# Optimization experiments

Hardware: AMD Instinct MI355X
Metric: run time of the kernel (lower is better)

## Reference

```python
import jax, jax.numpy as jnp
import numpy as np
import math
from jax import lax

N_SCALES = 5
ORDER = 2
INC, OUTC = 20, 40
MIN = np.arange(N_SCALES) * 0.2          # per-scale band lower edges [0,.2,.4,.6,.8]
MAX = MIN + 0.2                          # per-scale band upper edges [.2,...,1.0]
SIGMA0 = (MIN + MAX) / 2.0               # sigma at init (scales=0 -> tanh=0)
FS = [int(math.ceil(2.0 * s)) for s in SIGMA0]  # static half filter sizes [1,1,1,2,2]
MAXK = 2 * max(FS) + 1                   # padded kernel size (5)


def _hermite_derivs(x, sigma, order):
    # n-th Gaussian derivative: (-1/(sigma*sqrt2))^n * H_n(x/(sigma*sqrt2)) * g(x)
    g = jnp.exp(-(x ** 2) / (2.0 * sigma ** 2))
    g = g / jnp.sum(g)  # unit-sum normalized Gaussian envelope
    u = x / (sigma * math.sqrt(2.0))
    H = [jnp.ones_like(u), 2.0 * u]
    for n in range(1, order):
        H.append(2.0 * u * H[n] - 2.0 * n * H[n - 1])
    return [((-1.0 / (sigma * math.sqrt(2.0))) ** n) * H[n] * g for n in range(order + 1)]


def _basis(x, sigma, order):
    # 2D separable Gaussian-Hermite basis, all (i,j) with i+j <= order -> [N,k,k]
    d = _hermite_derivs(x, sigma, order)
    return jnp.stack([jnp.outer(d[i], d[j])
                      for i in range(order + 1) for j in range(order + 1 - i)])


def _make_filters(alphas, scales):
    mn = jnp.asarray(MIN, jnp.float32)
    mx = jnp.asarray(MAX, jnp.float32)
    sigma = (mx - mn) / 2.0 * jnp.tanh(scales) + (mn + mx) / 2.0  # learn_sigma=True path
    filts = []
    for s in range(N_SCALES):
        x = jnp.arange(-FS[s], FS[s] + 1, dtype=jnp.float32)
        B = _basis(x, sigma[s], ORDER)                    # [N, k, k]
        f = jnp.einsum('nkl,nio->oikl', B, alphas[s])     # [outC/ns, inC/ns, k, k]
        p = (MAXK - (2 * FS[s] + 1)) // 2                 # zero-pad to common size
        f = jnp.pad(f, ((0, 0), (0, 0), (p, p), (p, p)))
        filts.append(f)
    return jnp.concatenate(filts, axis=0)                 # [outC, inC/ns, K, K]


def setup_inputs() -> dict:
    key = jax.random.key(0)
    k1, k2 = jax.random.split(key)
    n_basis = (ORDER + 1) * (ORDER + 2) // 2  # 6
    data = jax.random.normal(k1, (16, INC, 384, 384), dtype=jnp.float32)
    alphas = jax.random.normal(k2, (N_SCALES, n_basis, INC // N_SCALES, OUTC // N_SCALES), dtype=jnp.float32)
    scales = jnp.zeros((N_SCALES,), dtype=jnp.float32)
    return {"data": data, "alphas": alphas, "scales": scales}


def reference(data, alphas, scales):
    w = _make_filters(alphas, scales)
    pad = MAXK // 2
    return lax.conv_general_dilated(
        data, w, window_strides=(1, 1), padding=[(pad, pad), (pad, pad)],
        dimension_numbers=('NCHW', 'OIHW', 'NCHW'),
        feature_group_count=N_SCALES)
```

## Files before the change

### kernel.cpp

```cpp
#include <hip/hip_runtime.h>
#include <math.h>

#define BATCH 16
#define G 5
#define CI 4
#define CO 8
#define HW 384
#define KK 5
#define PADD 2

typedef float v2f __attribute__((ext_vector_type(2)));

__global__ void gen_weights(const float* __restrict__ alphas,
                            const float* __restrict__ scales,
                            float* __restrict__ w) {
    int idx = blockIdx.x * blockDim.x + threadIdx.x;
    if (idx >= G * CI * KK * KK) return;
    int kx = idx % 5; int r = idx / 5;
    int ky = r % 5;   r /= 5;
    int i  = r % 4;   int s = r / 4;

    float mn = 0.2f * (float)s;
    float mx = mn + 0.2f;
    float sigma = 0.5f * (mx - mn) * tanhf(scales[s]) + 0.5f * (mn + mx);
    int fs = (s < 3) ? 1 : 2;
    int p  = 2 - fs;

    float outw[CO];
    bool valid = (ky >= p) && (ky < 5 - p) && (kx >= p) && (kx < 5 - p);
    if (!valid) {
        #pragma unroll
        for (int o = 0; o < CO; ++o) outw[o] = 0.f;
    } else {
        float inv2s2 = 1.f / (2.f * sigma * sigma);
        float Gs = 0.f;
        for (int t = -fs; t <= fs; ++t) Gs += expf(-(float)(t * t) * inv2s2);
        const float sqrt2 = 1.41421356237309505f;
        float c = -1.f / (sigma * sqrt2);

        float xy = (float)(ky - p - fs);
        float xx = (float)(kx - p - fs);

        float gy = expf(-xy * xy * inv2s2) / Gs;
        float gx = expf(-xx * xx * inv2s2) / Gs;
        float uy = xy / (sigma * sqrt2);
        float ux = xx / (sigma * sqrt2);

        float dy[3], dx[3];
        dy[0] = gy;
        dy[1] = c * 2.f * uy * gy;
        dy[2] = c * c * (4.f * uy * uy - 2.f) * gy;
        dx[0] = gx;
        dx[1] = c * 2.f * ux * gx;
        dx[2] = c * c * (4.f * ux * ux - 2.f) * gx;

        float bas[6];
        bas[0] = dy[0] * dx[0];
        bas[1] = dy[0] * dx[1];
        bas[2] = dy[0] * dx[2];
        bas[3] = dy[1] * dx[0];
        bas[4] = dy[1] * dx[1];
        bas[5] = dy[2] * dx[0];

        #pragma unroll
        for (int o = 0; o < CO; ++o) {
            float acc = 0.f;
            #pragma unroll
            for (int n = 0; n < 6; ++n)
                acc += bas[n] * alphas[((s * 6 + n) * CI + i) * CO + o];
            outw[o] = acc;
        }
    }
    float* dst = w + ((((s * CI + i) * KK + ky) * KK + kx) * CO);
    #pragma unroll
    for (int o = 0; o < CO; ++o) dst[o] = outw[o];
}

#define TLE 32
#define IT 36

__global__ __launch_bounds__(256) void conv_kernel(const float* __restrict__ in,
                                                   const float* __restrict__ w,
                                                   float* __restrict__ out) {
    __shared__ float s_in[CI][IT][IT];

    const int tileX = blockIdx.x * TLE;
    const int tileY = blockIdx.y * TLE;
    const int bz = blockIdx.z;
    const int g = bz % G;
    const int b = bz / G;
    const int tid = threadIdx.x;

    const float* inb = in + ((size_t)b * (G * CI) + g * CI) * (HW * HW);
    for (int l = tid; l < CI * IT * IT; l += 256) {
        int c = l / (IT * IT);
        int r = l - c * (IT * IT);
        int ly = r / IT;
        int lx = r - ly * IT;
        int gy = tileY - PADD + ly;
        int gx = tileX - PADD + lx;
        float v = 0.f;
        if ((unsigned)gy < (unsigned)HW && (unsigned)gx < (unsigned)HW)
            v = inb[c * (HW * HW) + gy * HW + gx];
        s_in[c][ly][lx] = v;
    }
    __syncthreads();

    const int xc = tid & 7;
    const int ty = tid >> 3;
    const int xl0 = xc * 4;

    v2f acc[4][4];
    #pragma unroll
    for (int op = 0; op < 4; ++op)
        #pragma unroll
        for (int x = 0; x < 4; ++x) acc[op][x] = (v2f)0.f;

    const v2f* wg = (const v2f*)(w + (size_t)g * (CI * KK * KK * CO));

    for (int i = 0; i < CI; ++i) {
        #pragma unroll
        for (int ky = 0; ky < KK; ++ky) {
            const float* row = &s_in[i][ty + ky][xl0];
            float4 a0 = *(const float4*)(row);
            float4 a1 = *(const float4*)(row + 4);
            float iv[8] = {a0.x, a0.y, a0.z, a0.w, a1.x, a1.y, a1.z, a1.w};

            const v2f* wrow = wg + (size_t)(i * (KK * KK) + ky * KK) * 4;
            #pragma unroll
            for (int kx = 0; kx < KK; ++kx) {
                v2f W0 = wrow[kx * 4 + 0];
                v2f W1 = wrow[kx * 4 + 1];
                v2f W2 = wrow[kx * 4 + 2];
                v2f W3 = wrow[kx * 4 + 3];
                #pragma unroll
                for (int x = 0; x < 4; ++x) {
                    const int t = kx + x;
                    v2f pv = {iv[t], iv[t]};
                    acc[0][x] += W0 * pv;
                    acc[1][x] += W1 * pv;
                    acc[2][x] += W2 * pv;
                    acc[3][x] += W3 * pv;
                }
            }
        }
    }

    const int oy = tileY + ty;
    float* outb = out + (((size_t)b * (G * CO) + g * CO) * HW + oy) * HW + tileX + xl0;
    #pragma unroll
    for (int o = 0; o < CO; ++o) {
        float4 rr;
        rr.x = acc[o >> 1][0][o & 1];
        rr.y = acc[o >> 1][1][o & 1];
        rr.z = acc[o >> 1][2][o & 1];
        rr.w = acc[o >> 1][3][o & 1];
        *(float4*)(outb + (size_t)o * (HW * HW)) = rr;
    }
}

extern "C" void kernel_launch(void* const* d_in, const int* in_sizes, int n_in,
                              void* d_out, int out_size, void* d_ws, size_t ws_size,
                              hipStream_t stream) {
    const float* data   = (const float*)d_in[0];
    const float* alphas = (const float*)d_in[1];
    const float* scales = (const float*)d_in[2];
    float* out = (float*)d_out;
    float* w   = (float*)d_ws;

    gen_weights<<<2, 256, 0, stream>>>(alphas, scales, w);

    dim3 grid(HW / TLE, HW / TLE, BATCH * G);
    conv_kernel<<<grid, 256, 0, stream>>>(data, w, out);
}
```

Before: 622.0 us.

## Exploit separable Gaussian-Hermite basis: vertical pass to shared fp16, then horizontal plus alpha mix

Replaces the dense 5x5 grouped convolution with a separable form. Each block first applies the three 1D vertical derivative filters per input channel and stores the results in shared memory as fp16. It then applies the horizontal filters and mixes the six basis responses into eight outputs using alphas. This cuts FLOPs per output substantially. In exchange it adds a second shared-memory stage and sync, and storing intermediates in half precision risks accuracy loss.

```diff
diff --git a/kernel.cpp b/kernel.cpp
--- a/kernel.cpp
+++ b/kernel.cpp
@@ -6,83 +6,46 @@
 #define CI 4
 #define CO 8
 #define HW 384
-#define KK 5
 #define PADD 2
+#define TLE 32
+#define IT 36
 
-typedef float v2f __attribute__((ext_vector_type(2)));
+typedef _Float16 h2 __attribute__((ext_vector_type(2)));
 
-__global__ void gen_weights(const float* __restrict__ alphas,
-                            const float* __restrict__ scales,
-                            float* __restrict__ w) {
+__global__ void gen_dtable(const float* __restrict__ scales, float* __restrict__ d) {
     int idx = blockIdx.x * blockDim.x + threadIdx.x;
-    if (idx >= G * CI * KK * KK) return;
-    int kx = idx % 5; int r = idx / 5;
-    int ky = r % 5;   r /= 5;
-    int i  = r % 4;   int s = r / 4;
+    if (idx >= G * 15) return;
+    int tap = idx % 5; int r = idx / 5;
+    int di = r % 3;    int s = r / 3;
 
     float mn = 0.2f * (float)s;
     float mx = mn + 0.2f;
     float sigma = 0.5f * (mx - mn) * tanhf(scales[s]) + 0.5f * (mn + mx);
     int fs = (s < 3) ? 1 : 2;
-    int p  = 2 - fs;
+    int x = tap - 2;
 
-    float outw[CO];
-    bool valid = (ky >= p) && (ky < 5 - p) && (kx >= p) && (kx < 5 - p);
-    if (!valid) {
-        #pragma unroll
-        for (int o = 0; o < CO; ++o) outw[o] = 0.f;
-    } else {
+    float val = 0.f;
+    if (x >= -fs && x <= fs) {
         float inv2s2 = 1.f / (2.f * sigma * sigma);
         float Gs = 0.f;
         for (int t = -fs; t <= fs; ++t) Gs += expf(-(float)(t * t) * inv2s2);
+        float gg = expf(-(float)(x * x) * inv2s2) / Gs;
         const float sqrt2 = 1.41421356237309505f;
         float c = -1.f / (sigma * sqrt2);
-
-        float xy = (float)(ky - p - fs);
-        float xx = (float)(kx - p - fs);
-
-        float gy = expf(-xy * xy * inv2s2) / Gs;
-        float gx = expf(-xx * xx * inv2s2) / Gs;
-        float uy = xy / (sigma * sqrt2);
-        float ux = xx / (sigma * sqrt2);
-
-        float dy[3], dx[3];
-        dy[0] = gy;
-        dy[1] = c * 2.f * uy * gy;
-        dy[2] = c * c * (4.f * uy * uy - 2.f) * gy;
-        dx[0] = gx;
-        dx[1] = c * 2.f * ux * gx;
-        dx[2] = c * c * (4.f * ux * ux - 2.f) * gx;
-
-        float bas[6];
-        bas[0] = dy[0] * dx[0];
-        bas[1] = dy[0] * dx[1];
-        bas[2] = dy[0] * dx[2];
-        bas[3] = dy[1] * dx[0];
-        bas[4] = dy[1] * dx[1];
-        bas[5] = dy[2] * dx[0];
-
-        #pragma unroll
-        for (int o = 0; o < CO; ++o) {
-            float acc = 0.f;
-            #pragma unroll
-            for (int n = 0; n < 6; ++n)
-                acc += bas[n] * alphas[((s * 6 + n) * CI + i) * CO + o];
-            outw[o] = acc;
-        }
+        float u = (float)x / (sigma * sqrt2);
+        if (di == 0)      val = gg;
+        else if (di == 1) val = c * 2.f * u * gg;
+        else              val = c * c * (4.f * u * u - 2.f) * gg;
     }
-    float* dst = w + ((((s * CI + i) * KK + ky) * KK + kx) * CO);
-    #pragma unroll
-    for (int o = 0; o < CO; ++o) dst[o] = outw[o];
+    d[(s * 3 + di) * 5 + tap] = val;
 }
 
-#define TLE 32
-#define IT 36
-
 __global__ __launch_bounds__(256) void conv_kernel(const float* __restrict__ in,
-                                                   const float* __restrict__ w,
+                                                   const float* __restrict__ dt,
+                                                   const float* __restrict__ alphas,
                                                    float* __restrict__ out) {
     __shared__ float s_in[CI][IT][IT];
+    __shared__ unsigned short s_v[CI * 3][TLE][IT];
 
     const int tileX = blockIdx.x * TLE;
     const int tileY = blockIdx.y * TLE;
@@ -104,43 +67,89 @@
             v = inb[c * (HW * HW) + gy * HW + gx];
         s_in[c][ly][lx] = v;
     }
+
+    float D[3][5];
+    {
+        const float* dg = dt + g * 15;
+        #pragma unroll
+        for (int di = 0; di < 3; ++di)
+            #pragma unroll
+            for (int t = 0; t < 5; ++t) D[di][t] = dg[di * 5 + t];
+    }
+    __syncthreads();
+
+    #pragma unroll
+    for (int rnd = 0; rnd < 2; ++rnd) {
+        int s = tid + rnd * 256;
+        if (s < 288) {
+            int y = (s * 57) >> 9;
+            int q = s - y * 9;
+            #pragma unroll
+            for (int i = 0; i < CI; ++i) {
+                float4 rr[5];
+                #pragma unroll
+                for (int r = 0; r < 5; ++r)
+                    rr[r] = *(const float4*)&s_in[i][y + r][q * 4];
+                #pragma unroll
+                for (int di = 0; di < 3; ++di) {
+                    float v0 = 0.f, v1 = 0.f, v2 = 0.f, v3 = 0.f;
+                    #pragma unroll
+                    for (int r = 0; r < 5; ++r) {
+                        v0 += D[di][r] * rr[r].x;
+                        v1 += D[di][r] * rr[r].y;
+                        v2 += D[di][r] * rr[r].z;
+                        v3 += D[di][r] * rr[r].w;
+                    }
+                    union { uint2 u2; h2 h[2]; } cv;
+                    cv.h[0][0] = (_Float16)v0; cv.h[0][1] = (_Float16)v1;
+                    cv.h[1][0] = (_Float16)v2; cv.h[1][1] = (_Float16)v3;
+                    *(uint2*)&s_v[i * 3 + di][y][q * 4] = cv.u2;
+                }
+            }
+        }
+    }
     __syncthreads();
 
     const int xc = tid & 7;
     const int ty = tid >> 3;
     const int xl0 = xc * 4;
 
-    v2f acc[4][4];
+    float acc[CO][4];
     #pragma unroll
-    for (int op = 0; op < 4; ++op)
+    for (int o = 0; o < CO; ++o)
         #pragma unroll
-        for (int x = 0; x < 4; ++x) acc[op][x] = (v2f)0.f;
+        for (int e = 0; e < 4; ++e) acc[o][e] = 0.f;
 
-    const v2f* wg = (const v2f*)(w + (size_t)g * (CI * KK * KK * CO));
+    const float* al = alphas + (size_t)g * (6 * CI * CO);
 
     for (int i = 0; i < CI; ++i) {
         #pragma unroll
-        for (int ky = 0; ky < KK; ++ky) {
-            const float* row = &s_in[i][ty + ky][xl0];
-            float4 a0 = *(const float4*)(row);
-            float4 a1 = *(const float4*)(row + 4);
-            float iv[8] = {a0.x, a0.y, a0.z, a0.w, a1.x, a1.y, a1.z, a1.w};
-
-            const v2f* wrow = wg + (size_t)(i * (KK * KK) + ky * KK) * 4;
+        for (int di = 0; di < 3; ++di) {
+            union { uint2 u2; h2 h[2]; } c0, c1;
+            c0.u2 = *(const uint2*)&s_v[i * 3 + di][ty][xl0];
+            c1.u2 = *(const uint2*)&s_v[i * 3 + di][ty][xl0 + 4];
+            float uu[8];
+            uu[0] = (float)c0.h[0][0]; uu[1] = (float)c0.h[0][1];
+            uu[2] = (float)c0.h[1][0]; uu[3] = (float)c0.h[1][1];
+            uu[4] = (float)c1.h[0][0]; uu[5] = (float)c1.h[0][1];
+            uu[6] = (float)c1.h[1][0]; uu[7] = (float)c1.h[1][1];
             #pragma unroll
-            for (int kx = 0; kx < KK; ++kx) {
-                v2f W0 = wrow[kx * 4 + 0];
-                v2f W1 = wrow[kx * 4 + 1];
-                v2f W2 = wrow[kx * 4 + 2];
-                v2f W3 = wrow[kx * 4 + 3];
+            for (int dj = 0; dj < 3 - di; ++dj) {
+                const int n = (di == 0) ? dj : ((di == 1) ? 3 + dj : 5);
+                float yv[4];
                 #pragma unroll
-                for (int x = 0; x < 4; ++x) {
-                    const int t = kx + x;
-                    v2f pv = {iv[t], iv[t]};
-                    acc[0][x] += W0 * pv;
-                    acc[1][x] += W1 * pv;
-                    acc[2][x] += W2 * pv;
-                    acc[3][x] += W3 * pv;
+                for (int e = 0; e < 4; ++e) {
+                    float a = 0.f;
+                    #pragma unroll
+                    for (int kx = 0; kx < 5; ++kx) a += D[dj][kx] * uu[e + kx];
+                    yv[e] = a;
+                }
+                const float* a8 = al + (n * CI + i) * CO;
+                #pragma unroll
+                for (int o = 0; o < CO; ++o) {
+                    float wv = a8[o];
+                    #pragma unroll
+                    for (int e = 0; e < 4; ++e) acc[o][e] += wv * yv[e];
                 }
             }
         }
@@ -151,10 +160,10 @@
     #pragma unroll
     for (int o = 0; o < CO; ++o) {
         float4 rr;
-        rr.x = acc[o >> 1][0][o & 1];
-        rr.y = acc[o >> 1][1][o & 1];
-        rr.z = acc[o >> 1][2][o & 1];
-        rr.w = acc[o >> 1][3][o & 1];
+        rr.x = acc[o][0];
+        rr.y = acc[o][1];
+        rr.z = acc[o][2];
+        rr.w = acc[o][3];
         *(float4*)(outb + (size_t)o * (HW * HW)) = rr;
     }
 }
@@ -166,10 +175,10 @@
     const float* alphas = (const float*)d_in[1];
     const float* scales = (const float*)d_in[2];
     float* out = (float*)d_out;
-    float* w   = (float*)d_ws;
+    float* dt  = (float*)d_ws;
 
-    gen_weights<<<2, 256, 0, stream>>>(alphas, scales, w);
+    gen_dtable<<<1, 128, 0, stream>>>(scales, dt);
 
     dim3 grid(HW / TLE, HW / TLE, BATCH * G);
-    conv_kernel<<<grid, 256, 0, stream>>>(data, w, out);
+    conv_kernel<<<grid, 256, 0, stream>>>(data, dt, alphas, out);
 }
```

New measurement: 688.6 us. +10.7%, slower.
